# Performance work log

Hardware: AMD Instinct MI355X
Metric: run time of the kernel (lower is better)

Reference implementation:

```python
import jax, jax.numpy as jnp
import numpy as np

B, N, D, H, F, L = 4, 1024, 1024, 16, 4096, 4  # batch, seq(nin), d_model, heads, d_ff, blocks
DH = D // H
STD = 0.02
LN_EPS = 1e-5
NEG = 1e10


def _layernorm(x, scale, shift):
    mean = x.mean(-1, keepdims=True)
    var = ((x - mean) ** 2).mean(-1, keepdims=True)
    return scale * ((x - mean) * jax.lax.rsqrt(var + LN_EPS)) + shift


def _gelu(x):
    # tanh-approx GeLU as in the source GeLU module
    c = np.sqrt(2.0 / np.pi).astype(np.float32)
    return 0.5 * x * (1.0 + jnp.tanh(c * (x + 0.044715 * x * x * x)))


def setup_inputs() -> dict:
    key = jax.random.key(0)
    ks = jax.random.split(key, 8)
    x = jax.random.normal(ks[0], (B, N, D), dtype=jnp.float32)
    mask_f = jnp.tril(jnp.ones((N, N), jnp.float32))  # i >= j causal mask, MASK_SCHEME=0
    return {
        "x": x,
        "mask_f": mask_f,
        "ln1_scale": jnp.ones((L, D), jnp.float32),
        "ln1_shift": jnp.zeros((L, D), jnp.float32),
        "qkv_w": jax.random.normal(ks[1], (L, D, 3 * D), jnp.float32) * STD,
        "qkv_b": jnp.zeros((L, 3 * D), jnp.float32),
        "out_w": jax.random.normal(ks[2], (L, D, D), jnp.float32) * STD,
        "out_b": jnp.zeros((L, D), jnp.float32),
        "ln2_scale": jnp.ones((L, D), jnp.float32),
        "ln2_shift": jnp.zeros((L, D), jnp.float32),
        "mlp_w1": jax.random.normal(ks[3], (L, D, F), jnp.float32) * STD,
        "mlp_b1": jnp.zeros((L, F), jnp.float32),
        "mlp_w2": jax.random.normal(ks[4], (L, F, D), jnp.float32) * STD,
        "mlp_b2": jnp.zeros((L, D), jnp.float32),
    }


def _block(x, mask_f, ln1_s, ln1_b, qkv_w, qkv_b, out_w, out_b,
           ln2_s, ln2_b, w1, b1, w2, b2):
    # attention sub-block (do_residual=True since MASK_SCHEME==0)
    residual = x
    h = _layernorm(x, ln1_s, ln1_b)
    qkv = h @ qkv_w + qkv_b                       # [B,N,3D]
    q, k, v = jnp.split(qkv, 3, axis=-1)
    def heads(t):                                  # [B,N,D] -> [B,H,N,DH]
        return t.reshape(B, N, H, DH).transpose(0, 2, 1, 3)
    q, k, v = heads(q), heads(k), heads(v)
    scores = jnp.einsum("bhqd,bhkd->bhqk", q, k) / np.sqrt(DH).astype(np.float32)
    scores = scores * mask_f - (1.0 - mask_f) * NEG
    attn = jax.nn.softmax(scores, axis=-1)
    o = jnp.einsum("bhqk,bhkd->bhqd", attn, v)     # [B,H,N,DH]
    o = o.transpose(0, 2, 1, 3).reshape(B, N, D)
    x = residual + (o @ out_w + out_b)
    # MLP sub-block
    residual = x
    h = _layernorm(x, ln2_s, ln2_b)
    x = residual + (_gelu(h @ w1 + b1) @ w2 + b2)
    return x


def reference(x, mask_f, ln1_scale, ln1_shift, qkv_w, qkv_b, out_w, out_b,
              ln2_scale, ln2_shift, mlp_w1, mlp_b1, mlp_w2, mlp_b2):
    for i in range(L):
        x = _block(x, mask_f, ln1_scale[i], ln1_shift[i], qkv_w[i], qkv_b[i],
                   out_w[i], out_b[i], ln2_scale[i], ln2_shift[i],
                   mlp_w1[i], mlp_b1[i], mlp_w2[i], mlp_b2[i])
    return x
```

## Files before the change

kernel.cpp:

```cpp
#include <hip/hip_runtime.h>
#include <cstdint>
#include <cstddef>


#define D_MODEL 1024
#define SEQ     1024
#define BATCH   4
#define HEADS   16
#define DHEAD   64
#define DFF     4096
#define LAYERS  4

typedef unsigned short u16;
typedef __attribute__((ext_vector_type(8))) short s16x8;
typedef __attribute__((ext_vector_type(4))) float f32x4;
typedef __attribute__((ext_vector_type(4))) unsigned short u16x4;

__device__ __forceinline__ u16 bf16_rn(float x) {
  uint32_t u = __float_as_uint(x);
  uint32_t r = (u + 0x7fffu + ((u >> 16) & 1u)) >> 16;
  return (u16)r;
}
__device__ __forceinline__ float bf16_f(u16 h) {
  return __uint_as_float((uint32_t)h << 16);
}
__device__ __forceinline__ void split2(float x, u16& hi, u16& lo) {
  hi = bf16_rn(x);
  lo = bf16_rn(x - bf16_f(hi));
}
__device__ __forceinline__ size_t split_addr(int x, int kk, int KT) {
  return ((size_t)(x >> 7) * KT + (kk >> 5)) * 4096 +
         (size_t)(((kk >> 3) & 3) * 1024 + (x & 127) * 8 + (kk & 7));
}
__device__ __forceinline__ int xcd_swz_lin(int lin, int nwg) {
  return (lin & 7) * (nwg >> 3) + (lin >> 3);
}

#define GLDS(gp, lp)                                                           \
  __builtin_amdgcn_global_load_lds(                                            \
      (const __attribute__((address_space(1))) uint32_t*)(gp),                 \
      (__attribute__((address_space(3))) uint32_t*)(lp), 16, 0, 0)

__global__ __launch_bounds__(256, 4) void wsplit_kernel(
    const float* __restrict__ W, u16* __restrict__ whi, u16* __restrict__ wlo,
    int K, int N)
{
  __shared__ float L[32][129];
  const int kt = blockIdx.x, nt = blockIdx.y;
  const int t = threadIdx.x;
  {
    const int k = t >> 3, nq = (t & 7) * 16;
    const float* src = W + (size_t)(kt * 32 + k) * N + nt * 128 + nq;
#pragma unroll
    for (int i2 = 0; i2 < 4; ++i2) {
      float4 v = *(const float4*)(src + i2 * 4);
      L[k][nq + i2 * 4 + 0] = v.x; L[k][nq + i2 * 4 + 1] = v.y;
      L[k][nq + i2 * 4 + 2] = v.z; L[k][nq + i2 * 4 + 3] = v.w;
    }
  }
  __syncthreads();
  const int n = t & 127, kr0 = t >> 7;
  const size_t tile = ((size_t)nt * (K >> 5) + kt) * 4096;
#pragma unroll
  for (int rr = kr0; rr < 4; rr += 2) {
    s16x8 hv, lv;
#pragma unroll
    for (int j = 0; j < 8; ++j) {
      float x = L[rr * 8 + j][n];
      u16 h_, l_; split2(x, h_, l_);
      hv[j] = (short)h_; lv[j] = (short)l_;
    }
    size_t ad = tile + (size_t)rr * 1024 + (size_t)n * 8;
    *(s16x8*)(whi + ad) = hv;
    *(s16x8*)(wlo + ad) = lv;
  }
}

__global__ __launch_bounds__(256, 8) void ln_split_kernel(
    const float* __restrict__ x, const float* __restrict__ scale,
    const float* __restrict__ shift, u16* __restrict__ hhi, u16* __restrict__ hlo)
{
  const int row = blockIdx.x;
  const int tid = threadIdx.x;
  const float* xr = x + (size_t)row * D_MODEL;
  float4 v = *(const float4*)(xr + tid * 4);
  float s  = v.x + v.y + v.z + v.w;
  float s2 = v.x * v.x + v.y * v.y + v.z * v.z + v.w * v.w;
  for (int o = 32; o; o >>= 1) {
    s  += __shfl_xor(s,  o, 64);
    s2 += __shfl_xor(s2, o, 64);
  }
  __shared__ float rb[8];
  int wave = tid >> 6, lane = tid & 63;
  if (lane == 0) { rb[wave] = s; rb[4 + wave] = s2; }
  __syncthreads();
  float S  = rb[0] + rb[1] + rb[2] + rb[3];
  float S2 = rb[4] + rb[5] + rb[6] + rb[7];
  float mean = S * (1.0f / D_MODEL);
  float var  = S2 * (1.0f / D_MODEL) - mean * mean;
  float rstd = rsqrtf(var + 1e-5f);
  float4 sc = *(const float4*)(scale + tid * 4);
  float4 sh = *(const float4*)(shift + tid * 4);
  float y0 = sc.x * (v.x - mean) * rstd + sh.x;
  float y1 = sc.y * (v.y - mean) * rstd + sh.y;
  float y2 = sc.z * (v.z - mean) * rstd + sh.z;
  float y3 = sc.w * (v.w - mean) * rstd + sh.w;
  int c0 = tid * 4;
  size_t ad = split_addr(row, c0, D_MODEL / 32);
  u16 h0, l0, h1, l1, h2, l2, h3, l3;
  split2(y0, h0, l0); split2(y1, h1, l1);
  split2(y2, h2, l2); split2(y3, h3, l3);
  u16x4 hv = {h0, h1, h2, h3};
  u16x4 lv = {l0, l1, l2, l3};
  *(u16x4*)(hhi + ad) = hv;
  *(u16x4*)(hlo + ad) = lv;
}

enum { EPI_QKV = 0, EPI_RES = 1, EPI_GELU = 2 };

template <int EPI>
__global__ __launch_bounds__(256, 2) void gemm_split(
    const u16* __restrict__ Ah_g, const u16* __restrict__ Al_g,
    const u16* __restrict__ Bh_g, const u16* __restrict__ Bl_g,
    const float* __restrict__ bias, float* __restrict__ C,
    int N, int KT,
    u16* __restrict__ qhb, u16* __restrict__ qlb,
    u16* __restrict__ khb, u16* __restrict__ klb,
    u16* __restrict__ vthb, u16* __restrict__ vtlb,
    u16* __restrict__ ghi, u16* __restrict__ glo)
{
  __shared__ u16 smem[2][4][4096];
  const int tid = threadIdx.x, w = tid >> 6, lane = tid & 63;
  const int wr = w >> 1, wc = w & 1;
  const int g4 = lane >> 4, l16 = lane & 15;
  const int nbx = gridDim.x;
  const int lin = blockIdx.y * nbx + blockIdx.x;
  const int swz = xcd_swz_lin(lin, nbx * gridDim.y);
  const int bx = swz % nbx, by = swz / nbx;

  f32x4 acc[4][4];
#pragma unroll
  for (int i = 0; i < 4; ++i)
#pragma unroll
    for (int j = 0; j < 4; ++j) acc[i][j] = (f32x4){0.f, 0.f, 0.f, 0.f};

  const size_t tA0 = (size_t)by * KT, tB0 = (size_t)bx * KT;

#define GSTAGE(bufi, kti) do {                                                 \
    const char* _gAh = (const char*)(Ah_g + (tA0 + (kti)) * 4096);             \
    const char* _gAl = (const char*)(Al_g + (tA0 + (kti)) * 4096);             \
    const char* _gBh = (const char*)(Bh_g + (tB0 + (kti)) * 4096);             \
    const char* _gBl = (const char*)(Bl_g + (tB0 + (kti)) * 4096);             \
    _Pragma("unroll")                                                          \
    for (int _i = 0; _i < 2; ++_i) {                                           \
      const int _ofs = (w * 2 + _i) * 1024;                                    \
      const int _lofs = _ofs + lane * 16;                                      \
      GLDS(_gAh + _lofs, (char*)smem[bufi][0] + _ofs);                         \
      GLDS(_gAl + _lofs, (char*)smem[bufi][1] + _ofs);                         \
      GLDS(_gBh + _lofs, (char*)smem[bufi][2] + _ofs);                         \
      GLDS(_gBl + _lofs, (char*)smem[bufi][3] + _ofs);                         \
    }                                                                          \
  } while (0)

  GSTAGE(0, 0);
  __syncthreads();
  for (int kt = 0; kt < KT; ++kt) {
    const int cur = kt & 1;
    if (kt + 1 < KT) GSTAGE(cur ^ 1, kt + 1);

    const u16* sAh = smem[cur][0];
    const u16* sAl = smem[cur][1];
    const u16* sBh = smem[cur][2];
    const u16* sBl = smem[cur][3];
    s16x8 ah[4], al[4], bh[4], bl[4];
    const int ab = g4 * 1024 + (wr * 64 + l16) * 8;
    const int bb = g4 * 1024 + (wc * 64 + l16) * 8;
#pragma unroll
    for (int mf = 0; mf < 4; ++mf) {
      ah[mf] = *(const s16x8*)(sAh + ab + mf * 128);
      al[mf] = *(const s16x8*)(sAl + ab + mf * 128);
    }
#pragma unroll
    for (int nf = 0; nf < 4; ++nf) {
      bh[nf] = *(const s16x8*)(sBh + bb + nf * 128);
      bl[nf] = *(const s16x8*)(sBl + bb + nf * 128);
    }
#pragma unroll
    for (int mf = 0; mf < 4; ++mf)
#pragma unroll
      for (int nf = 0; nf < 4; ++nf) {
        acc[mf][nf] = __builtin_amdgcn_mfma_f32_16x16x32_bf16(
            ah[mf], bh[nf], acc[mf][nf], 0, 0, 0);
        acc[mf][nf] = __builtin_amdgcn_mfma_f32_16x16x32_bf16(
            ah[mf], bl[nf], acc[mf][nf], 0, 0, 0);
        acc[mf][nf] = __builtin_amdgcn_mfma_f32_16x16x32_bf16(
            al[mf], bh[nf], acc[mf][nf], 0, 0, 0);
      }
    __syncthreads();
  }
#undef GSTAGE

  const int r0 = by * 128 + wr * 64;
  const int c0 = bx * 128 + wc * 64;
#pragma unroll
  for (int mf = 0; mf < 4; ++mf) {
#pragma unroll
    for (int nf = 0; nf < 4; ++nf) {
      const int c = c0 + nf * 16 + l16;
      const float bv = bias[c];
#pragma unroll
      for (int reg = 0; reg < 4; ++reg) {
        const int r = r0 + mf * 16 + g4 * 4 + reg;
        float val = acc[mf][nf][reg] + bv;
        if (EPI == EPI_QKV) {
          int b_ = r >> 10, n_ = r & (SEQ - 1);
          int part = c >> 10, cc = c & (D_MODEL - 1);
          int head = cc >> 6, dd = cc & (DHEAD - 1);
          int bh_ = b_ * HEADS + head;
          u16 h_, l_; split2(val, h_, l_);
          size_t base = ((size_t)bh_ * 16 + (n_ >> 6)) * 4096;
          if (part == 0) {
            size_t ad = base + (dd >> 3) * 512 + (n_ & 63) * 8 + (dd & 7);
            qhb[ad] = h_; qlb[ad] = l_;
          } else if (part == 1) {
            size_t ad = base + (dd >> 3) * 512 + (n_ & 63) * 8 + (dd & 7);
            khb[ad] = h_; klb[ad] = l_;
          } else {
            size_t ad = base + ((n_ & 63) >> 3) * 512 + dd * 8 + (n_ & 7);
            vthb[ad] = h_; vtlb[ad] = l_;
          }
        } else if (EPI == EPI_RES) {
          C[(size_t)r * D_MODEL + c] += val;
        } else {
          float u = val;
          float z = 1.5957691216057308f * (u + 0.044715f * u * u * u);
          float gv = u / (1.0f + __expf(-z));
          u16 h_, l_; split2(gv, h_, l_);
          size_t ad = split_addr(r, c, DFF / 32);
          ghi[ad] = h_; glo[ad] = l_;
        }
      }
    }
  }
}

__global__ __launch_bounds__(256, 2) void attn_mfma(
    const u16* __restrict__ qh, const u16* __restrict__ ql,
    const u16* __restrict__ kh, const u16* __restrict__ kl,
    const u16* __restrict__ vth, const u16* __restrict__ vtl,
    u16* __restrict__ ohi, u16* __restrict__ olo)
{
  __shared__ u16 skv[2][4][4096];
  __shared__ u16 pbuf[4][16 * 72];

  const int tid = threadIdx.x, w = tid >> 6, lane = tid & 63;
  const int g4 = lane >> 4, l16 = lane & 15;
  const int swzb = xcd_swz_lin(blockIdx.x, gridDim.x);
  const int bh = swzb >> 4, qt = swzb & 15;

  const size_t tq = ((size_t)bh * 16 + qt) * 4096;
  s16x8 qhf[2], qlf[2];
#pragma unroll
  for (int g = 0; g < 2; ++g) {
    const int ad = (g * 4 + g4) * 512 + (w * 16 + l16) * 8;
    qhf[g] = *(const s16x8*)(qh + tq + ad);
    qlf[g] = *(const s16x8*)(ql + tq + ad);
  }

  f32x4 acc[4];
#pragma unroll
  for (int df = 0; df < 4; ++df) acc[df] = (f32x4){0.f, 0.f, 0.f, 0.f};
  float m[4] = {-3.0e38f, -3.0e38f, -3.0e38f, -3.0e38f};
  float l[4] = {0.f, 0.f, 0.f, 0.f};

#define KVSTAGE(bufi, kti) do {                                                \
    const size_t _tk = ((size_t)bh * 16 + (kti)) * 4096;                       \
    _Pragma("unroll")                                                          \
    for (int _i = 0; _i < 2; ++_i) {                                           \
      const int _ofs = (w * 2 + _i) * 1024;                                    \
      const int _lofs = _ofs + lane * 16;                                      \
      GLDS((const char*)(kh + _tk) + _lofs, (char*)skv[bufi][0] + _ofs);       \
      GLDS((const char*)(kl + _tk) + _lofs, (char*)skv[bufi][1] + _ofs);       \
      GLDS((const char*)(vth + _tk) + _lofs, (char*)skv[bufi][2] + _ofs);      \
      GLDS((const char*)(vtl + _tk) + _lofs, (char*)skv[bufi][3] + _ofs);      \
    }                                                                          \
  } while (0)

  KVSTAGE(0, 0);
  __syncthreads();
  for (int kt = 0; kt <= qt; ++kt) {
    const int cur = kt & 1;
    if (kt < qt) KVSTAGE(cur ^ 1, kt + 1);

    const u16* skh = skv[cur][0];
    const u16* skl = skv[cur][1];
    f32x4 s[4];
#pragma unroll
    for (int nf = 0; nf < 4; ++nf) {
      s[nf] = (f32x4){0.f, 0.f, 0.f, 0.f};
#pragma unroll
      for (int g = 0; g < 2; ++g) {
        const int kb = (g * 4 + g4) * 512 + (nf * 16 + l16) * 8;
        s16x8 khf = *(const s16x8*)(skh + kb);
        s16x8 klf = *(const s16x8*)(skl + kb);
        s[nf] = __builtin_amdgcn_mfma_f32_16x16x32_bf16(qhf[g], khf, s[nf], 0, 0, 0);
        s[nf] = __builtin_amdgcn_mfma_f32_16x16x32_bf16(qhf[g], klf, s[nf], 0, 0, 0);
        s[nf] = __builtin_amdgcn_mfma_f32_16x16x32_bf16(qlf[g], khf, s[nf], 0, 0, 0);
      }
    }
    const bool diag = (kt == qt);
    const int qloc = w * 16 + g4 * 4;
#pragma unroll
    for (int nf = 0; nf < 4; ++nf) {
      const int keyl = nf * 16 + l16;
#pragma unroll
      for (int r = 0; r < 4; ++r) {
        float sv = s[nf][r] * 0.125f;
        if (diag && keyl > qloc + r) sv = -1.0e10f;
        s[nf][r] = sv;
      }
    }
    float corr[4];
#pragma unroll
    for (int r = 0; r < 4; ++r) {
      float sv = fmaxf(fmaxf(s[0][r], s[1][r]), fmaxf(s[2][r], s[3][r]));
      sv = fmaxf(sv, __shfl_xor(sv, 1, 64));
      sv = fmaxf(sv, __shfl_xor(sv, 2, 64));
      sv = fmaxf(sv, __shfl_xor(sv, 4, 64));
      sv = fmaxf(sv, __shfl_xor(sv, 8, 64));
      float mn = fmaxf(m[r], sv);
      corr[r] = __expf(m[r] - mn);
      m[r] = mn;
    }
#pragma unroll
    for (int nf = 0; nf < 4; ++nf)
#pragma unroll
      for (int r = 0; r < 4; ++r)
        s[nf][r] = __expf(s[nf][r] - m[r]);
#pragma unroll
    for (int r = 0; r < 4; ++r) {
      float ps = s[0][r] + s[1][r] + s[2][r] + s[3][r];
      ps += __shfl_xor(ps, 1, 64);
      ps += __shfl_xor(ps, 2, 64);
      ps += __shfl_xor(ps, 4, 64);
      ps += __shfl_xor(ps, 8, 64);
      l[r] = l[r] * corr[r] + ps;
    }
#pragma unroll
    for (int df = 0; df < 4; ++df)
#pragma unroll
      for (int r = 0; r < 4; ++r)
        acc[df][r] *= corr[r];

    u16* pb = pbuf[w];
#pragma unroll
    for (int nf = 0; nf < 4; ++nf)
#pragma unroll
      for (int r = 0; r < 4; ++r)
        pb[(g4 * 4 + r) * 72 + nf * 16 + l16] = bf16_rn(s[nf][r]);
    __syncthreads();
    s16x8 pa[2];
#pragma unroll
    for (int g = 0; g < 2; ++g)
      pa[g] = *(const s16x8*)(pb + l16 * 72 + g * 32 + g4 * 8);

    const u16* svh = skv[cur][2];
    const u16* svl = skv[cur][3];
#pragma unroll
    for (int df = 0; df < 4; ++df)
#pragma unroll
      for (int g = 0; g < 2; ++g) {
        const int vb_ = (g * 4 + g4) * 512 + (df * 16 + l16) * 8;
        s16x8 vhf = *(const s16x8*)(svh + vb_);
        s16x8 vlf = *(const s16x8*)(svl + vb_);
        acc[df] = __builtin_amdgcn_mfma_f32_16x16x32_bf16(pa[g], vhf, acc[df], 0, 0, 0);
        acc[df] = __builtin_amdgcn_mfma_f32_16x16x32_bf16(pa[g], vlf, acc[df], 0, 0, 0);
      }
    __syncthreads();
  }
#undef KVSTAGE

  const int b_ = bh >> 4, h_ = bh & 15;
#pragma unroll
  for (int df = 0; df < 4; ++df) {
    const int c = h_ * 64 + df * 16 + l16;
#pragma unroll
    for (int r = 0; r < 4; ++r) {
      const int n_ = qt * 64 + w * 16 + g4 * 4 + r;
      float val = acc[df][r] / l[r];
      u16 h2, l2; split2(val, h2, l2);
      size_t ad = split_addr(b_ * SEQ + n_, c, D_MODEL / 32);
      ohi[ad] = h2; olo[ad] = l2;
    }
  }
}

extern "C" void kernel_launch(void* const* d_in, const int* in_sizes, int n_in,
                              void* d_out, int out_size, void* d_ws, size_t ws_size,
                              hipStream_t stream)
{
  const float* x_in  = (const float*)d_in[0];
  const float* ln1_s = (const float*)d_in[2];
  const float* ln1_b = (const float*)d_in[3];
  const float* qkv_w = (const float*)d_in[4];
  const float* qkv_b = (const float*)d_in[5];
  const float* out_w = (const float*)d_in[6];
  const float* out_b = (const float*)d_in[7];
  const float* ln2_s = (const float*)d_in[8];
  const float* ln2_b = (const float*)d_in[9];
  const float* w1    = (const float*)d_in[10];
  const float* b1    = (const float*)d_in[11];
  const float* w2    = (const float*)d_in[12];
  const float* b2    = (const float*)d_in[13];

  float* x = (float*)d_out;
  char* wsb = (char*)d_ws;
  const size_t MB = (size_t)1 << 20;
  const size_t MEG = (size_t)1 << 20;
  u16* whi = (u16*)(wsb + 0);
  u16* wlo = (u16*)(wsb + 24 * MB);
  u16* hhi = (u16*)(wsb + 48 * MB);
  u16* hlo = (u16*)(wsb + 56 * MB);
  u16* ohi = (u16*)(wsb + 64 * MB);
  u16* olo = (u16*)(wsb + 72 * MB);
  u16* qhb  = (u16*)(wsb + 80 * MB);
  u16* qlb  = (u16*)(wsb + 88 * MB);
  u16* khb  = (u16*)(wsb + 96 * MB);
  u16* klb  = (u16*)(wsb + 104 * MB);
  u16* vthb = (u16*)(wsb + 112 * MB);
  u16* vtlb = (u16*)(wsb + 120 * MB);
  u16* ghi = (u16*)(wsb + 80 * MB);
  u16* glo = (u16*)(wsb + 112 * MB);

  const size_t OQKV = 0, OOUT = 3 * MEG, OW1 = 4 * MEG, OW2 = 8 * MEG;
  const int T = BATCH * SEQ;

  (void)hipMemcpyAsync(x, x_in, (size_t)T * D_MODEL * sizeof(float),
                       hipMemcpyDeviceToDevice, stream);

  for (int lyr = 0; lyr < LAYERS; ++lyr) {
    wsplit_kernel<<<dim3(32, 24), 256, 0, stream>>>(
        qkv_w + (size_t)lyr * D_MODEL * 3 * D_MODEL, whi + OQKV, wlo + OQKV,
        D_MODEL, 3 * D_MODEL);
    wsplit_kernel<<<dim3(32, 8), 256, 0, stream>>>(
        out_w + (size_t)lyr * D_MODEL * D_MODEL, whi + OOUT, wlo + OOUT,
        D_MODEL, D_MODEL);
    wsplit_kernel<<<dim3(32, 32), 256, 0, stream>>>(
        w1 + (size_t)lyr * D_MODEL * DFF, whi + OW1, wlo + OW1,
        D_MODEL, DFF);
    wsplit_kernel<<<dim3(128, 8), 256, 0, stream>>>(
        w2 + (size_t)lyr * DFF * D_MODEL, whi + OW2, wlo + OW2,
        DFF, D_MODEL);

    ln_split_kernel<<<T, 256, 0, stream>>>(x, ln1_s + lyr * D_MODEL,
                                           ln1_b + lyr * D_MODEL, hhi, hlo);
    gemm_split<EPI_QKV><<<dim3(24, 32), 256, 0, stream>>>(
        hhi, hlo, whi + OQKV, wlo + OQKV,
        qkv_b + (size_t)lyr * 3 * D_MODEL, nullptr,
        3 * D_MODEL, D_MODEL / 32,
        qhb, qlb, khb, klb, vthb, vtlb, nullptr, nullptr);
    attn_mfma<<<BATCH * HEADS * (SEQ / 64), 256, 0, stream>>>(
        qhb, qlb, khb, klb, vthb, vtlb, ohi, olo);
    gemm_split<EPI_RES><<<dim3(8, 32), 256, 0, stream>>>(
        ohi, olo, whi + OOUT, wlo + OOUT,
        out_b + (size_t)lyr * D_MODEL, x,
        D_MODEL, D_MODEL / 32,
        nullptr, nullptr, nullptr, nullptr, nullptr, nullptr, nullptr, nullptr);

    ln_split_kernel<<<T, 256, 0, stream>>>(x, ln2_s + lyr * D_MODEL,
                                           ln2_b + lyr * D_MODEL, hhi, hlo);
    gemm_split<EPI_GELU><<<dim3(32, 32), 256, 0, stream>>>(
        hhi, hlo, whi + OW1, wlo + OW1,
        b1 + (size_t)lyr * DFF, nullptr,
        DFF, D_MODEL / 32,
        nullptr, nullptr, nullptr, nullptr, nullptr, nullptr, ghi, glo);
    gemm_split<EPI_RES><<<dim3(8, 32), 256, 0, stream>>>(
        ghi, glo, whi + OW2, wlo + OW2,
        b2 + (size_t)lyr * D_MODEL, x,
        D_MODEL, DFF / 32,
        nullptr, nullptr, nullptr, nullptr, nullptr, nullptr, nullptr, nullptr);
  }
}
```

Baseline: 1.951 ms.

## Drop weight low-part term in split GEMMs and process two query tiles per attention block

Weights are now rounded to a single bf16 part, so the split GEMMs use two MFMA terms (Ah*Bh + Al*Bh) instead of three. This cuts B-tile loads, LDS and MFMA work by about a third, and raises the occupancy target to 3 blocks per SM. The attention kernel now handles two adjacent query tiles per block and shares each K/V stage between them, halving the grid and reusing K/V traffic. Dropping the weight low part lowers GEMM accuracy, and pairing query tiles may unbalance the causal workload.

```diff
diff --git a/kernel.cpp b/kernel.cpp
--- a/kernel.cpp
+++ b/kernel.cpp
@@ -42,8 +42,7 @@
       (__attribute__((address_space(3))) uint32_t*)(lp), 16, 0, 0)
 
 __global__ __launch_bounds__(256, 4) void wsplit_kernel(
-    const float* __restrict__ W, u16* __restrict__ whi, u16* __restrict__ wlo,
-    int K, int N)
+    const float* __restrict__ W, u16* __restrict__ whi, int K, int N)
 {
   __shared__ float L[32][129];
   const int kt = blockIdx.x, nt = blockIdx.y;
@@ -63,16 +62,10 @@
   const size_t tile = ((size_t)nt * (K >> 5) + kt) * 4096;
 #pragma unroll
   for (int rr = kr0; rr < 4; rr += 2) {
-    s16x8 hv, lv;
-#pragma unroll
-    for (int j = 0; j < 8; ++j) {
-      float x = L[rr * 8 + j][n];
-      u16 h_, l_; split2(x, h_, l_);
-      hv[j] = (short)h_; lv[j] = (short)l_;
-    }
-    size_t ad = tile + (size_t)rr * 1024 + (size_t)n * 8;
-    *(s16x8*)(whi + ad) = hv;
-    *(s16x8*)(wlo + ad) = lv;
+    s16x8 hv;
+#pragma unroll
+    for (int j = 0; j < 8; ++j) hv[j] = (short)bf16_rn(L[rr * 8 + j][n]);
+    *(s16x8*)(whi + tile + (size_t)rr * 1024 + (size_t)n * 8) = hv;
   }
 }
 
@@ -118,8 +111,8 @@
 
 enum { EPI_QKV = 0, EPI_RES = 1, EPI_GELU = 2 };
 
-template <int EPI>
-__global__ __launch_bounds__(256, 2) void gemm_split(
+template <int EPI, int TERMS>
+__global__ __launch_bounds__(256, 3) void gemm_split(
     const u16* __restrict__ Ah_g, const u16* __restrict__ Al_g,
     const u16* __restrict__ Bh_g, const u16* __restrict__ Bl_g,
     const float* __restrict__ bias, float* __restrict__ C,
@@ -129,7 +122,7 @@
     u16* __restrict__ vthb, u16* __restrict__ vtlb,
     u16* __restrict__ ghi, u16* __restrict__ glo)
 {
-  __shared__ u16 smem[2][4][4096];
+  __shared__ u16 smem[2][(TERMS == 3) ? 4 : 3][4096];
   const int tid = threadIdx.x, w = tid >> 6, lane = tid & 63;
   const int wr = w >> 1, wc = w & 1;
   const int g4 = lane >> 4, l16 = lane & 15;
@@ -150,7 +143,6 @@
     const char* _gAh = (const char*)(Ah_g + (tA0 + (kti)) * 4096);             \
     const char* _gAl = (const char*)(Al_g + (tA0 + (kti)) * 4096);             \
     const char* _gBh = (const char*)(Bh_g + (tB0 + (kti)) * 4096);             \
-    const char* _gBl = (const char*)(Bl_g + (tB0 + (kti)) * 4096);             \
     _Pragma("unroll")                                                          \
     for (int _i = 0; _i < 2; ++_i) {                                           \
       const int _ofs = (w * 2 + _i) * 1024;                                    \
@@ -158,7 +150,10 @@
       GLDS(_gAh + _lofs, (char*)smem[bufi][0] + _ofs);                         \
       GLDS(_gAl + _lofs, (char*)smem[bufi][1] + _ofs);                         \
       GLDS(_gBh + _lofs, (char*)smem[bufi][2] + _ofs);                         \
-      GLDS(_gBl + _lofs, (char*)smem[bufi][3] + _ofs);                         \
+      if (TERMS == 3) {                                                        \
+        const char* _gBl = (const char*)(Bl_g + (tB0 + (kti)) * 4096);         \
+        GLDS(_gBl + _lofs, (char*)smem[bufi][TERMS] + _ofs);                   \
+      }                                                                        \
     }                                                                          \
   } while (0)
 
@@ -171,8 +166,7 @@
     const u16* sAh = smem[cur][0];
     const u16* sAl = smem[cur][1];
     const u16* sBh = smem[cur][2];
-    const u16* sBl = smem[cur][3];
-    s16x8 ah[4], al[4], bh[4], bl[4];
+    s16x8 ah[4], al[4], bh[4];
     const int ab = g4 * 1024 + (wr * 64 + l16) * 8;
     const int bb = g4 * 1024 + (wc * 64 + l16) * 8;
 #pragma unroll
@@ -181,10 +175,8 @@
       al[mf] = *(const s16x8*)(sAl + ab + mf * 128);
     }
 #pragma unroll
-    for (int nf = 0; nf < 4; ++nf) {
+    for (int nf = 0; nf < 4; ++nf)
       bh[nf] = *(const s16x8*)(sBh + bb + nf * 128);
-      bl[nf] = *(const s16x8*)(sBl + bb + nf * 128);
-    }
 #pragma unroll
     for (int mf = 0; mf < 4; ++mf)
 #pragma unroll
@@ -192,9 +184,13 @@
         acc[mf][nf] = __builtin_amdgcn_mfma_f32_16x16x32_bf16(
             ah[mf], bh[nf], acc[mf][nf], 0, 0, 0);
         acc[mf][nf] = __builtin_amdgcn_mfma_f32_16x16x32_bf16(
-            ah[mf], bl[nf], acc[mf][nf], 0, 0, 0);
-        acc[mf][nf] = __builtin_amdgcn_mfma_f32_16x16x32_bf16(
             al[mf], bh[nf], acc[mf][nf], 0, 0, 0);
+        if (TERMS == 3) {
+          const u16* sBl = smem[cur][TERMS == 3 ? 3 : 2];
+          s16x8 bl = *(const s16x8*)(sBl + bb + nf * 128);
+          acc[mf][nf] = __builtin_amdgcn_mfma_f32_16x16x32_bf16(
+              ah[mf], bl, acc[mf][nf], 0, 0, 0);
+        }
       }
     __syncthreads();
   }
@@ -256,22 +252,33 @@
   const int tid = threadIdx.x, w = tid >> 6, lane = tid & 63;
   const int g4 = lane >> 4, l16 = lane & 15;
   const int swzb = xcd_swz_lin(blockIdx.x, gridDim.x);
-  const int bh = swzb >> 4, qt = swzb & 15;
-
-  const size_t tq = ((size_t)bh * 16 + qt) * 4096;
-  s16x8 qhf[2], qlf[2];
-#pragma unroll
-  for (int g = 0; g < 2; ++g) {
-    const int ad = (g * 4 + g4) * 512 + (w * 16 + l16) * 8;
-    qhf[g] = *(const s16x8*)(qh + tq + ad);
-    qlf[g] = *(const s16x8*)(ql + tq + ad);
-  }
-
-  f32x4 acc[4];
-#pragma unroll
-  for (int df = 0; df < 4; ++df) acc[df] = (f32x4){0.f, 0.f, 0.f, 0.f};
-  float m[4] = {-3.0e38f, -3.0e38f, -3.0e38f, -3.0e38f};
-  float l[4] = {0.f, 0.f, 0.f, 0.f};
+  const int bh = swzb >> 3, qt2 = swzb & 7;
+  const int qta = qt2 * 2, qtb = qt2 * 2 + 1;
+
+  s16x8 qhfA[2], qlfA[2], qhfB[2], qlfB[2];
+  {
+    const size_t tqa = ((size_t)bh * 16 + qta) * 4096;
+    const size_t tqb = ((size_t)bh * 16 + qtb) * 4096;
+#pragma unroll
+    for (int g = 0; g < 2; ++g) {
+      const int ad = (g * 4 + g4) * 512 + (w * 16 + l16) * 8;
+      qhfA[g] = *(const s16x8*)(qh + tqa + ad);
+      qlfA[g] = *(const s16x8*)(ql + tqa + ad);
+      qhfB[g] = *(const s16x8*)(qh + tqb + ad);
+      qlfB[g] = *(const s16x8*)(ql + tqb + ad);
+    }
+  }
+
+  f32x4 accA[4], accB[4];
+#pragma unroll
+  for (int df = 0; df < 4; ++df) {
+    accA[df] = (f32x4){0.f, 0.f, 0.f, 0.f};
+    accB[df] = (f32x4){0.f, 0.f, 0.f, 0.f};
+  }
+  float mA[4] = {-3.0e38f, -3.0e38f, -3.0e38f, -3.0e38f};
+  float lA[4] = {0.f, 0.f, 0.f, 0.f};
+  float mB[4] = {-3.0e38f, -3.0e38f, -3.0e38f, -3.0e38f};
+  float lB[4] = {0.f, 0.f, 0.f, 0.f};
 
 #define KVSTAGE(bufi, kti) do {                                                \
     const size_t _tk = ((size_t)bh * 16 + (kti)) * 4096;                       \
@@ -286,99 +293,104 @@
     }                                                                          \
   } while (0)
 
+#define PROCESS(QHF, QLF, ACC, MM, LL, DIAG) do {                              \
+    f32x4 s[4];                                                                \
+    _Pragma("unroll")                                                          \
+    for (int nf = 0; nf < 4; ++nf) {                                           \
+      s[nf] = (f32x4){0.f, 0.f, 0.f, 0.f};                                     \
+      _Pragma("unroll")                                                        \
+      for (int g = 0; g < 2; ++g) {                                            \
+        const int kb = (g * 4 + g4) * 512 + (nf * 16 + l16) * 8;               \
+        s16x8 khf = *(const s16x8*)(skh + kb);                                 \
+        s16x8 klf = *(const s16x8*)(skl + kb);                                 \
+        s[nf] = __builtin_amdgcn_mfma_f32_16x16x32_bf16(QHF[g], khf, s[nf], 0, 0, 0); \
+        s[nf] = __builtin_amdgcn_mfma_f32_16x16x32_bf16(QHF[g], klf, s[nf], 0, 0, 0); \
+        s[nf] = __builtin_amdgcn_mfma_f32_16x16x32_bf16(QLF[g], khf, s[nf], 0, 0, 0); \
+      }                                                                        \
+    }                                                                          \
+    const int qloc = w * 16 + g4 * 4;                                          \
+    _Pragma("unroll")                                                          \
+    for (int nf = 0; nf < 4; ++nf) {                                           \
+      const int keyl = nf * 16 + l16;                                          \
+      _Pragma("unroll")                                                        \
+      for (int r = 0; r < 4; ++r) {                                            \
+        float sv = s[nf][r] * 0.125f;                                          \
+        if ((DIAG) && keyl > qloc + r) sv = -1.0e10f;                          \
+        s[nf][r] = sv;                                                         \
+      }                                                                        \
+    }                                                                          \
+    float corr[4];                                                             \
+    _Pragma("unroll")                                                          \
+    for (int r = 0; r < 4; ++r) {                                              \
+      float sv = fmaxf(fmaxf(s[0][r], s[1][r]), fmaxf(s[2][r], s[3][r]));      \
+      sv = fmaxf(sv, __shfl_xor(sv, 1, 64));                                   \
+      sv = fmaxf(sv, __shfl_xor(sv, 2, 64));                                   \
+      sv = fmaxf(sv, __shfl_xor(sv, 4, 64));                                   \
+      sv = fmaxf(sv, __shfl_xor(sv, 8, 64));                                   \
+      float mn = fmaxf(MM[r], sv);                                             \
+      corr[r] = __expf(MM[r] - mn);                                            \
+      MM[r] = mn;                                                              \
+    }                                                                          \
+    _Pragma("unroll")                                                          \
+    for (int nf = 0; nf < 4; ++nf)                                             \
+      _Pragma("unroll")                                                        \
+      for (int r = 0; r < 4; ++r)                                              \
+        s[nf][r] = __expf(s[nf][r] - MM[r]);                                   \
+    _Pragma("unroll")                                                          \
+    for (int r = 0; r < 4; ++r) {                                              \
+      float ps = s[0][r] + s[1][r] + s[2][r] + s[3][r];                        \
+      ps += __shfl_xor(ps, 1, 64);                                             \
+      ps += __shfl_xor(ps, 2, 64);                                             \
+      ps += __shfl_xor(ps, 4, 64);                                             \
+      ps += __shfl_xor(ps, 8, 64);                                             \
+      LL[r] = LL[r] * corr[r] + ps;                                            \
+    }                                                                          \
+    _Pragma("unroll")                                                          \
+    for (int df = 0; df < 4; ++df)                                             \
+      _Pragma("unroll")                                                        \
+      for (int r = 0; r < 4; ++r)                                              \
+        ACC[df][r] *= corr[r];                                                 \
+    u16* pb = pbuf[w];                                                         \
+    _Pragma("unroll")                                                          \
+    for (int nf = 0; nf < 4; ++nf)                                             \
+      _Pragma("unroll")                                                        \
+      for (int r = 0; r < 4; ++r)                                              \
+        pb[(g4 * 4 + r) * 72 + nf * 16 + l16] = bf16_rn(s[nf][r]);             \
+    __syncthreads();                                                           \
+    s16x8 pa[2];                                                               \
+    _Pragma("unroll")                                                          \
+    for (int g = 0; g < 2; ++g)                                                \
+      pa[g] = *(const s16x8*)(pb + l16 * 72 + g * 32 + g4 * 8);                \
+    _Pragma("unroll")                                                          \
+    for (int df = 0; df < 4; ++df)                                             \
+      _Pragma("unroll")                                                        \
+      for (int g = 0; g < 2; ++g) {                                            \
+        const int vb_ = (g * 4 + g4) * 512 + (df * 16 + l16) * 8;              \
+        s16x8 vhf = *(const s16x8*)(svh + vb_);                                \
+        s16x8 vlf = *(const s16x8*)(svl + vb_);                                \
+        ACC[df] = __builtin_amdgcn_mfma_f32_16x16x32_bf16(pa[g], vhf, ACC[df], 0, 0, 0); \
+        ACC[df] = __builtin_amdgcn_mfma_f32_16x16x32_bf16(pa[g], vlf, ACC[df], 0, 0, 0); \
+      }                                                                        \
+  } while (0)
+
   KVSTAGE(0, 0);
   __syncthreads();
-  for (int kt = 0; kt <= qt; ++kt) {
+  for (int kt = 0; kt <= qtb; ++kt) {
     const int cur = kt & 1;
-    if (kt < qt) KVSTAGE(cur ^ 1, kt + 1);
+    if (kt < qtb) KVSTAGE(cur ^ 1, kt + 1);
 
     const u16* skh = skv[cur][0];
     const u16* skl = skv[cur][1];
-    f32x4 s[4];
-#pragma unroll
-    for (int nf = 0; nf < 4; ++nf) {
-      s[nf] = (f32x4){0.f, 0.f, 0.f, 0.f};
-#pragma unroll
-      for (int g = 0; g < 2; ++g) {
-        const int kb = (g * 4 + g4) * 512 + (nf * 16 + l16) * 8;
-        s16x8 khf = *(const s16x8*)(skh + kb);
-        s16x8 klf = *(const s16x8*)(skl + kb);
-        s[nf] = __builtin_amdgcn_mfma_f32_16x16x32_bf16(qhf[g], khf, s[nf], 0, 0, 0);
-        s[nf] = __builtin_amdgcn_mfma_f32_16x16x32_bf16(qhf[g], klf, s[nf], 0, 0, 0);
-        s[nf] = __builtin_amdgcn_mfma_f32_16x16x32_bf16(qlf[g], khf, s[nf], 0, 0, 0);
-      }
-    }
-    const bool diag = (kt == qt);
-    const int qloc = w * 16 + g4 * 4;
-#pragma unroll
-    for (int nf = 0; nf < 4; ++nf) {
-      const int keyl = nf * 16 + l16;
-#pragma unroll
-      for (int r = 0; r < 4; ++r) {
-        float sv = s[nf][r] * 0.125f;
-        if (diag && keyl > qloc + r) sv = -1.0e10f;
-        s[nf][r] = sv;
-      }
-    }
-    float corr[4];
-#pragma unroll
-    for (int r = 0; r < 4; ++r) {
-      float sv = fmaxf(fmaxf(s[0][r], s[1][r]), fmaxf(s[2][r], s[3][r]));
-      sv = fmaxf(sv, __shfl_xor(sv, 1, 64));
-      sv = fmaxf(sv, __shfl_xor(sv, 2, 64));
-      sv = fmaxf(sv, __shfl_xor(sv, 4, 64));
-      sv = fmaxf(sv, __shfl_xor(sv, 8, 64));
-      float mn = fmaxf(m[r], sv);
-      corr[r] = __expf(m[r] - mn);
-      m[r] = mn;
-    }
-#pragma unroll
-    for (int nf = 0; nf < 4; ++nf)
-#pragma unroll
-      for (int r = 0; r < 4; ++r)
-        s[nf][r] = __expf(s[nf][r] - m[r]);
-#pragma unroll
-    for (int r = 0; r < 4; ++r) {
-      float ps = s[0][r] + s[1][r] + s[2][r] + s[3][r];
-      ps += __shfl_xor(ps, 1, 64);
-      ps += __shfl_xor(ps, 2, 64);
-      ps += __shfl_xor(ps, 4, 64);
-      ps += __shfl_xor(ps, 8, 64);
-      l[r] = l[r] * corr[r] + ps;
-    }
-#pragma unroll
-    for (int df = 0; df < 4; ++df)
-#pragma unroll
-      for (int r = 0; r < 4; ++r)
-        acc[df][r] *= corr[r];
-
-    u16* pb = pbuf[w];
-#pragma unroll
-    for (int nf = 0; nf < 4; ++nf)
-#pragma unroll
-      for (int r = 0; r < 4; ++r)
-        pb[(g4 * 4 + r) * 72 + nf * 16 + l16] = bf16_rn(s[nf][r]);
-    __syncthreads();
-    s16x8 pa[2];
-#pragma unroll
-    for (int g = 0; g < 2; ++g)
-      pa[g] = *(const s16x8*)(pb + l16 * 72 + g * 32 + g4 * 8);
-
     const u16* svh = skv[cur][2];
     const u16* svl = skv[cur][3];
-#pragma unroll
-    for (int df = 0; df < 4; ++df)
-#pragma unroll
-      for (int g = 0; g < 2; ++g) {
-        const int vb_ = (g * 4 + g4) * 512 + (df * 16 + l16) * 8;
-        s16x8 vhf = *(const s16x8*)(svh + vb_);
-        s16x8 vlf = *(const s16x8*)(svl + vb_);
-        acc[df] = __builtin_amdgcn_mfma_f32_16x16x32_bf16(pa[g], vhf, acc[df], 0, 0, 0);
-        acc[df] = __builtin_amdgcn_mfma_f32_16x16x32_bf16(pa[g], vlf, acc[df], 0, 0, 0);
-      }
+
+    if (kt <= qta)
+      PROCESS(qhfA, qlfA, accA, mA, lA, kt == qta);
+    PROCESS(qhfB, qlfB, accB, mB, lB, kt == qtb);
     __syncthreads();
   }
 #undef KVSTAGE
+#undef PROCESS
 
   const int b_ = bh >> 4, h_ = bh & 15;
 #pragma unroll
@@ -386,11 +398,21 @@
     const int c = h_ * 64 + df * 16 + l16;
 #pragma unroll
     for (int r = 0; r < 4; ++r) {
-      const int n_ = qt * 64 + w * 16 + g4 * 4 + r;
-      float val = acc[df][r] / l[r];
-      u16 h2, l2; split2(val, h2, l2);
-      size_t ad = split_addr(b_ * SEQ + n_, c, D_MODEL / 32);
-      ohi[ad] = h2; olo[ad] = l2;
+      const int rr = w * 16 + g4 * 4 + r;
+      {
+        const int n_ = qta * 64 + rr;
+        float val = accA[df][r] / lA[r];
+        u16 h2, l2; split2(val, h2, l2);
+        size_t ad = split_addr(b_ * SEQ + n_, c, D_MODEL / 32);
+        ohi[ad] = h2; olo[ad] = l2;
+      }
+      {
+        const int n_ = qtb * 64 + rr;
+        float val = accB[df][r] / lB[r];
+        u16 h2, l2; split2(val, h2, l2);
+        size_t ad = split_addr(b_ * SEQ + n_, c, D_MODEL / 32);
+        ohi[ad] = h2; olo[ad] = l2;
+      }
     }
   }
 }
@@ -418,7 +440,6 @@
   const size_t MB = (size_t)1 << 20;
   const size_t MEG = (size_t)1 << 20;
   u16* whi = (u16*)(wsb + 0);
-  u16* wlo = (u16*)(wsb + 24 * MB);
   u16* hhi = (u16*)(wsb + 48 * MB);
   u16* hlo = (u16*)(wsb + 56 * MB);
   u16* ohi = (u16*)(wsb + 64 * MB);
@@ -440,42 +461,42 @@
 
   for (int lyr = 0; lyr < LAYERS; ++lyr) {
     wsplit_kernel<<<dim3(32, 24), 256, 0, stream>>>(
-        qkv_w + (size_t)lyr * D_MODEL * 3 * D_MODEL, whi + OQKV, wlo + OQKV,
+        qkv_w + (size_t)lyr * D_MODEL * 3 * D_MODEL, whi + OQKV,
         D_MODEL, 3 * D_MODEL);
     wsplit_kernel<<<dim3(32, 8), 256, 0, stream>>>(
-        out_w + (size_t)lyr * D_MODEL * D_MODEL, whi + OOUT, wlo + OOUT,
+        out_w + (size_t)lyr * D_MODEL * D_MODEL, whi + OOUT,
         D_MODEL, D_MODEL);
     wsplit_kernel<<<dim3(32, 32), 256, 0, stream>>>(
-        w1 + (size_t)lyr * D_MODEL * DFF, whi + OW1, wlo + OW1,
+        w1 + (size_t)lyr * D_MODEL * DFF, whi + OW1,
         D_MODEL, DFF);
     wsplit_kernel<<<dim3(128, 8), 256, 0, stream>>>(
-        w2 + (size_t)lyr * DFF * D_MODEL, whi + OW2, wlo + OW2,
+        w2 + (size_t)lyr * DFF * D_MODEL, whi + OW2,
         DFF, D_MODEL);
 
     ln_split_kernel<<<T, 256, 0, stream>>>(x, ln1_s + lyr * D_MODEL,
                                            ln1_b + lyr * D_MODEL, hhi, hlo);
-    gemm_split<EPI_QKV><<<dim3(24, 32), 256, 0, stream>>>(
-        hhi, hlo, whi + OQKV, wlo + OQKV,
+    gemm_split<EPI_QKV, 2><<<dim3(24, 32), 256, 0, stream>>>(
+        hhi, hlo, whi + OQKV, nullptr,
         qkv_b + (size_t)lyr * 3 * D_MODEL, nullptr,
         3 * D_MODEL, D_MODEL / 32,
         qhb, qlb, khb, klb, vthb, vtlb, nullptr, nullptr);
-    attn_mfma<<<BATCH * HEADS * (SEQ / 64), 256, 0, stream>>>(
+    attn_mfma<<<BATCH * HEADS * (SEQ / 128), 256, 0, stream>>>(
         qhb, qlb, khb, klb, vthb, vtlb, ohi, olo);
-    gemm_split<EPI_RES><<<dim3(8, 32), 256, 0, stream>>>(
-        ohi, olo, whi + OOUT, wlo + OOUT,
+    gemm_split<EPI_RES, 2><<<dim3(8, 32), 256, 0, stream>>>(
+        ohi, olo, whi + OOUT, nullptr,
         out_b + (size_t)lyr * D_MODEL, x,
         D_MODEL, D_MODEL / 32,
         nullptr, nullptr, nullptr, nullptr, nullptr, nullptr, nullptr, nullptr);
 
     ln_split_kernel<<<T, 256, 0, stream>>>(x, ln2_s + lyr * D_MODEL,
                                            ln2_b + lyr * D_MODEL, hhi, hlo);
-    gemm_split<EPI_GELU><<<dim3(32, 32), 256, 0, stream>>>(
-        hhi, hlo, whi + OW1, wlo + OW1,
+    gemm_split<EPI_GELU, 2><<<dim3(32, 32), 256, 0, stream>>>(
+        hhi, hlo, whi + OW1, nullptr,
         b1 + (size_t)lyr * DFF, nullptr,
         DFF, D_MODEL / 32,
         nullptr, nullptr, nullptr, nullptr, nullptr, nullptr, ghi, glo);
-    gemm_split<EPI_RES><<<dim3(8, 32), 256, 0, stream>>>(
-        ghi, glo, whi + OW2, wlo + OW2,
+    gemm_split<EPI_RES, 2><<<dim3(8, 32), 256, 0, stream>>>(
+        ghi, glo, whi + OW2, nullptr,
         b2 + (size_t)lyr * D_MODEL, x,
         D_MODEL, DFF / 32,
         nullptr, nullptr, nullptr, nullptr, nullptr, nullptr, nullptr, nullptr);
```

New measurement: 1.599 ms. 18.0% less time.
